# Performance work log

Measured on AMD Instinct MI355X. Metric: run time of the kernel, lower is better.

## Reference

```python
import jax, jax.numpy as jnp
from jax import lax
import numpy as np

H = 128          # hidden_dim
VOCAB = 200000   # word_dim
L = 32           # words per node
NUM_LEAVES = 2048
NUM_PARENTS = 2047
MAXC = 4         # max child slots in a tree row
NCLASS = 4


def setup_inputs() -> dict:
    key = jax.random.key(0)
    ks = jax.random.split(key, 16)
    N = NUM_LEAVES + NUM_PARENTS
    x_word = jax.random.uniform(ks[0], (N, L), dtype=jnp.float32)
    x_index = jax.random.randint(ks[1], (N, L), 0, VOCAB)
    # caterpillar tree: parent idx has one leaf child and the previous parent
    idx = np.arange(NUM_PARENTS)
    tree = np.full((NUM_PARENTS, MAXC), -1, dtype=np.int32)
    tree[:, 0] = idx
    tree[:, 1] = np.where(idx > 0, NUM_LEAVES + idx - 1, NUM_LEAVES - 1)
    tree = jnp.asarray(tree)
    y = jax.random.uniform(ks[2], (NCLASS,), dtype=jnp.float32)
    def init(k, shp):
        return 0.1 * jax.random.normal(k, shp, dtype=jnp.float32)
    return dict(
        x_word=x_word, x_index=x_index, tree=tree, y=y,
        E_bu=init(ks[3], (H, VOCAB)),
        WQ=init(ks[4], (H, H)), WK=init(ks[5], (H, H)), WV=init(ks[6], (H, H)),
        W_z=init(ks[7], (H, H)), U_z=init(ks[8], (H, H)), b_z=jnp.zeros((H,), jnp.float32),
        W_r=init(ks[9], (H, H)), U_r=init(ks[10], (H, H)), b_r=jnp.zeros((H,), jnp.float32),
        W_h=init(ks[11], (H, H)), U_h=init(ks[12], (H, H)), b_h=jnp.zeros((H,), jnp.float32),
        W_out=init(ks[13], (NCLASS, H)), b_out=jnp.zeros((NCLASS,), jnp.float32),
    )


def _forward(x_word, y, E_bu, WQ, WK, WV, W_z, U_z, b_z, W_r, U_r, b_r,
             W_h, U_h, b_h, W_out, b_out, x_index, tree):
    Hd = E_bu.shape[0]
    # parent_xe for every node: weighted sum of embedding columns  [N, H]
    emb = E_bu.T[x_index]                        # [N, L, H] gather
    xe = jnp.einsum('nlh,nl->nh', emb, x_word)
    n_parents = tree.shape[0]
    n_leaves = x_word.shape[0] - n_parents

    def cell(xe_i, h_tilde):
        # W.mul(v).sum(dim=1) == W @ v in the torch code
        z = jax.nn.sigmoid(W_z @ xe_i + U_z @ h_tilde + b_z)
        r = jax.nn.sigmoid(W_r @ xe_i + U_r @ h_tilde + b_r)
        c = jnp.tanh(W_h @ xe_i + U_h @ (h_tilde * r) + b_h)
        return z * h_tilde + (1.0 - z) * c

    # leaves: child_h == 0  =>  h_tilde == 0 (vectorized over all leaves)
    xe_leaf = xe[:n_leaves]
    z_l = jax.nn.sigmoid(xe_leaf @ W_z.T + b_z)
    c_l = jnp.tanh(xe_leaf @ W_h.T + b_h)
    leaf_h = (1.0 - z_l) * c_l

    node_h0 = jnp.zeros((x_word.shape[0], Hd), xe.dtype).at[:n_leaves].set(leaf_h)
    scale = 1.0 / jnp.sqrt(jnp.asarray(Hd, xe.dtype))

    def step(node_h, inp):
        xe_p, row, i = inp
        mask = row >= 0
        child_h = node_h[jnp.clip(row, 0)]                  # [MAXC, H]
        query = jax.nn.sigmoid(xe_p @ WQ)                   # sigmoid(xe @ WQ)
        keyv = child_h @ WK
        val = child_h @ WV
        scores = jnp.where(mask, (query * scale * keyv).sum(-1), -1e9)
        attn = jax.nn.softmax(scores)                       # over children
        h_tilde = attn @ val
        h = cell(xe_p, h_tilde)
        return node_h.at[i].set(h), h

    idxs = jnp.arange(n_parents) + n_leaves
    _, parent_hs = lax.scan(step, node_h0, (xe[n_leaves:], tree, idxs))
    root = parent_hs[-1]
    pred = jax.nn.softmax(W_out @ root + b_out)
    loss = jnp.sum((y - pred) ** 2)
    return pred, loss


def reference(x_word, x_index, tree, y, E_bu, WQ, WK, WV, W_z, U_z, b_z,
              W_r, U_r, b_r, W_h, U_h, b_h, W_out, b_out):
    return _forward(x_word, y, E_bu, WQ, WK, WV, W_z, U_z, b_z, W_r, U_r, b_r,
                    W_h, U_h, b_h, W_out, b_out, x_index, tree)
```

## Files before the change

kernel.cpp:

```cpp
#include <hip/hip_runtime.h>
#include <math.h>

#define HD 128
#define LW 32
#define VOCABN 200000
#define NLEAF 2048
#define NPAR 2047
#define NNODE 4095
#define MAXC 4
#define NCLASS 4
#define SCALE 0.08838834764831845f

#define OFF_XE   0
#define OFF_NODE 524160
#define OFF_W3   786304
#define OFF_WQ   851840
#define OFF_AZ   1113856
#define OFF_AR   1375872
#define OFF_AH   1637888
#define OFF_PREV 1899904
#define OFF_ES   2685952
#define OFF_HG   2688000
#define OFF_HTR  2688128
#define OFF_ET   2688256
#define WS_END   (OFF_ET + (size_t)VOCABN * HD)

#define BARL() asm volatile("s_waitcnt lgkmcnt(0)\n\ts_barrier" ::: "memory")
#define PIN4(v) asm volatile("" : "+v"((v).x), "+v"((v).y), "+v"((v).z), "+v"((v).w))
#define LD4(p, k) (*(const float4*)((p) + 4 * (k)))

typedef __attribute__((ext_vector_type(16))) float fx16;

#define CH(W, X, n4) { a0 += (W).x * (X)[4*(n4)+0] + (W).y * (X)[4*(n4)+1]; \
                       a1 += (W).z * (X)[4*(n4)+2] + (W).w * (X)[4*(n4)+3]; }

#define PIN_ALL() do { PIN4(A0); PIN4(A1); PIN4(A2); PIN4(A3); \
    PIN4(A4); PIN4(A5); PIN4(A6); PIN4(A7); PIN4(A8); PIN4(A9); \
    PIN4(A10); PIN4(A11); PIN4(A12); PIN4(A13); PIN4(A14); PIN4(A15); } while (0)

__global__ void k_xe(const float* __restrict__ xw, const int* __restrict__ xi,
                     const float* __restrict__ E, float* __restrict__ xe) {
    int n = blockIdx.x;
    int h = threadIdx.x;
    __shared__ int   sidx[LW];
    __shared__ float sw[LW];
    if (h < LW) { sidx[h] = xi[n * LW + h]; sw[h] = xw[n * LW + h]; }
    __syncthreads();
    float acc = 0.f;
#pragma unroll
    for (int l = 0; l < LW; ++l)
        acc += E[(size_t)h * VOCABN + sidx[l]] * sw[l];
    xe[(size_t)n * HD + h] = acc;
}

__global__ void k_transpose(const float* __restrict__ E, float* __restrict__ ET) {
    __shared__ float tile[32][33];
    int vb = blockIdx.x * 32, hb = blockIdx.y * 32;
    int tx = threadIdx.x, ty = threadIdx.y;
#pragma unroll
    for (int r = 0; r < 32; r += 8)
        tile[ty + r][tx] = E[(size_t)(hb + ty + r) * VOCABN + vb + tx];
    __syncthreads();
#pragma unroll
    for (int r = 0; r < 32; r += 8)
        ET[(size_t)(vb + ty + r) * HD + hb + tx] = tile[tx][ty + r];
}

__global__ void k_xe_t(const float* __restrict__ xw, const int* __restrict__ xi,
                       const float* __restrict__ ET, float* __restrict__ xe) {
    int n = blockIdx.x;
    int h = threadIdx.x;
    __shared__ int   sidx[LW];
    __shared__ float sw[LW];
    if (h < LW) { sidx[h] = xi[n * LW + h]; sw[h] = xw[n * LW + h]; }
    __syncthreads();
    float acc = 0.f;
#pragma unroll
    for (int l = 0; l < LW; ++l)
        acc += ET[(size_t)sidx[l] * HD + h] * sw[l];
    xe[(size_t)n * HD + h] = acc;
}

__global__ void k_leaf(const float* __restrict__ xe, const float* __restrict__ Wz,
                       const float* __restrict__ bz, const float* __restrict__ Wh,
                       const float* __restrict__ bh, float* __restrict__ node_h) {
    int n = blockIdx.x;
    int j = threadIdx.x;
    __shared__ float xl[HD];
    xl[j] = xe[(size_t)n * HD + j];
    __syncthreads();
    float az = bz[j], ah = bh[j];
    const float* wzr = Wz + (size_t)j * HD;
    const float* whr = Wh + (size_t)j * HD;
#pragma unroll 4
    for (int k = 0; k < HD; ++k) { az += wzr[k] * xl[k]; ah += whr[k] * xl[k]; }
    float z = 1.f / (1.f + expf(-az));
    float c = tanhf(ah);
    node_h[(size_t)n * HD + j] = (1.f - z) * c;
}

__global__ void k_fuse(const float* __restrict__ WV, const float* __restrict__ Uz,
                       const float* __restrict__ Ur, const float* __restrict__ Uh,
                       float* __restrict__ w3) {
    int r = blockIdx.x;
    int b = threadIdx.x;
    float v;
    if (r < 128) {
        v = WV[(size_t)b * HD + r];
    } else if (r < 384) {
        const float* u  = (r < 256 ? Uz + (size_t)(r - 128) * HD : Ur + (size_t)(r - 256) * HD);
        const float* wv = WV + (size_t)b * HD;
        float a = 0.f;
#pragma unroll 4
        for (int j = 0; j < HD; ++j) a += u[j] * wv[j];
        v = a;
    } else {
        v = Uh[(size_t)(r - 384) * HD + b];
    }
    w3[(size_t)r * HD + b] = v;
}

__global__ void k_ppre(const float* __restrict__ xe, const float* __restrict__ WQ,
                       const float* __restrict__ WK, const float* __restrict__ Wz,
                       const float* __restrict__ bz, const float* __restrict__ Wr,
                       const float* __restrict__ br, const float* __restrict__ Wh,
                       const float* __restrict__ bh, float* __restrict__ wq,
                       float* __restrict__ az, float* __restrict__ ar,
                       float* __restrict__ ah) {
    int i = blockIdx.x;
    int j = threadIdx.x;
    __shared__ float xl[HD], ql[HD];
    xl[j] = xe[(size_t)(NLEAF + i) * HD + j];
    __syncthreads();
    float q = 0.f;
#pragma unroll 4
    for (int h = 0; h < HD; ++h) q += xl[h] * WQ[(size_t)h * HD + j];
    ql[j] = 1.f / (1.f + expf(-q));
    __syncthreads();
    float w = 0.f;
#pragma unroll 4
    for (int k = 0; k < HD; ++k) w += WK[(size_t)j * HD + k] * ql[k];
    wq[(size_t)i * HD + j] = w;
    float vz = bz[j], vr = br[j], vh = bh[j];
#pragma unroll 4
    for (int k = 0; k < HD; ++k) {
        float xv = xl[k];
        vz += Wz[(size_t)j * HD + k] * xv;
        vr += Wr[(size_t)j * HD + k] * xv;
        vh += Wh[(size_t)j * HD + k] * xv;
    }
    az[(size_t)i * HD + j] = vz;
    ar[(size_t)i * HD + j] = vr;
    ah[(size_t)i * HD + j] = vh;
}

__global__ void k_chpre(const int* __restrict__ tree, const float* __restrict__ node_h,
                        const float* __restrict__ w3, const float* __restrict__ wq_all,
                        float* __restrict__ preVexp, float* __restrict__ expsum) {
    int i = blockIdx.x;
    int j = threadIdx.x;
    __shared__ float hl[HD];
    __shared__ float red[HD];
    float wqj = wq_all[(size_t)i * HD + j];
    float acc0 = 0.f, acc1 = 0.f, acc2 = 0.f, esum = 0.f;
    for (int c = 0; c < MAXC; ++c) {
        int child = tree[i * MAXC + c];
        if (child < 0 || child >= NLEAF) continue;
        __syncthreads();
        hl[j] = node_h[(size_t)child * HD + j];
        __syncthreads();
        red[j] = hl[j] * wqj;
        __syncthreads();
        for (int s = 64; s > 0; s >>= 1) {
            if (j < s) red[j] += red[j + s];
            __syncthreads();
        }
        float e = expf(red[0] * SCALE);
        float d0 = 0.f, d1 = 0.f, d2 = 0.f;
#pragma unroll 4
        for (int k = 0; k < HD; ++k) {
            float x = hl[k];
            d0 += w3[(size_t)j * HD + k] * x;
            d1 += w3[(size_t)(128 + j) * HD + k] * x;
            d2 += w3[(size_t)(256 + j) * HD + k] * x;
        }
        acc0 += e * d0; acc1 += e * d1; acc2 += e * d2; esum += e;
    }
    preVexp[(size_t)i * 384 + j]       = acc0;
    preVexp[(size_t)i * 384 + 128 + j] = acc1;
    preVexp[(size_t)i * 384 + 256 + j] = acc2;
    if (j == 0) expsum[i] = esum;
}

__global__ __launch_bounds__(1024)
__attribute__((amdgpu_waves_per_eu(4, 4)))
void k_seq(float* __restrict__ ws, const float* __restrict__ Wout,
           const float* __restrict__ bout, const float* __restrict__ y,
           float* __restrict__ out) {
    const int t  = threadIdx.x;
    const int l  = t & 63;
    const int w  = t >> 6;
    const bool isP1 = (w < 12);
    const int q1   = w & 1;
    const int row1 = 64 * (w >> 1) + l;
    const int w12  = w - 12;
    const int q3   = w12 & 1;
    const int row3 = 64 * (w12 >> 1) + l;

    __shared__ float part1[768];
    __shared__ float part3[256];
    __shared__ float sPart[2];
    __shared__ float h_lds[HD];
    __shared__ float outv[NCLASS];

    const int woff = isP1 ? (row1 * HD + 64 * q1)
                          : ((384 + row3) * HD + 64 * q3);
    const float* wp = ws + OFF_W3 + woff;
    float4 A0 = LD4(wp, 0),  A1 = LD4(wp, 1),  A2 = LD4(wp, 2),  A3 = LD4(wp, 3),
           A4 = LD4(wp, 4),  A5 = LD4(wp, 5),  A6 = LD4(wp, 6),  A7 = LD4(wp, 7),
           A8 = LD4(wp, 8),  A9 = LD4(wp, 9),  A10 = LD4(wp, 10), A11 = LD4(wp, 11),
           A12 = LD4(wp, 12), A13 = LD4(wp, 13), A14 = LD4(wp, 14), A15 = LD4(wp, 15);
    PIN_ALL();

    const int xoff = isP1 ? (OFF_HG + 64 * q1) : (OFF_HTR + 64 * q3);
    const float* xp = ws + __builtin_amdgcn_readfirstlane(xoff);

    float pv0 = 0.f, pv1 = 0.f, pv2 = 0.f, paz = 0.f, par = 0.f, pah = 0.f,
          pwq = 0.f, pes = 0.f;
    if (t < HD) {
        pv0 = ws[OFF_PREV + t];       pv1 = ws[OFF_PREV + 128 + t];
        pv2 = ws[OFF_PREV + 256 + t];
        paz = ws[OFF_AZ + t];         par = ws[OFF_AR + t];
        pah = ws[OFF_AH + t];
        pwq = ws[OFF_WQ + HD + t];
        pes = ws[OFF_ES];
        ws[OFF_HG + t] = 0.f;
    }
    if (t < 2) sPart[t] = (t == 0) ? -1e30f : 0.f;
    asm volatile("s_waitcnt vmcnt(0)" ::: "memory");
    __syncthreads();

    float zreg = 0.f, htreg = 0.f, hfin = 0.f, cur_pah = 0.f, cur_pwq = 0.f;

    for (int i = 0; i < NPAR; ++i) {
        const int inext = (i + 1 < NPAR) ? i + 1 : NPAR - 1;
        const int in2   = (i + 2 < NPAR) ? i + 2 : NPAR - 1;

        PIN_ALL();

        if (isP1) {
            fx16 x0, x1, x2, x3;
            asm volatile(
                "s_dcache_inv\n\t"
                "s_load_dwordx16 %0, %4, 0x0\n\t"
                "s_load_dwordx16 %1, %4, 0x40\n\t"
                "s_load_dwordx16 %2, %4, 0x80\n\t"
                "s_load_dwordx16 %3, %4, 0xC0\n\t"
                "s_waitcnt lgkmcnt(0)"
                : "=s"(x0), "=s"(x1), "=s"(x2), "=s"(x3)
                : "s"(xp));
            float a0 = 0.f, a1 = 0.f;
            CH(A0, x0, 0)  CH(A1, x0, 1)  CH(A2, x0, 2)  CH(A3, x0, 3)
            CH(A4, x1, 0)  CH(A5, x1, 1)  CH(A6, x1, 2)  CH(A7, x1, 3)
            CH(A8, x2, 0)  CH(A9, x2, 1)  CH(A10, x2, 2) CH(A11, x2, 3)
            CH(A12, x3, 0) CH(A13, x3, 1) CH(A14, x3, 2) CH(A15, x3, 3)
            part1[q1 * 384 + row1] = a0 + a1;
        }
        BARL();

        if (t < HD) {
            float vdot = part1[t]       + part1[384 + t];
            float zdot = part1[128 + t] + part1[512 + t];
            float rdot = part1[256 + t] + part1[640 + t];
            float sc   = sPart[0] + sPart[1];
            float e    = expf(sc);
            float inv  = 1.f / (pes + e);
            float htv  = (pv0 + e * vdot) * inv;
            float z    = 1.f / (1.f + expf(-(paz + (pv1 + e * zdot) * inv)));
            float rr   = 1.f / (1.f + expf(-(par + (pv2 + e * rdot) * inv)));
            ws[OFF_HTR + t] = htv * rr;
            zreg = z; htreg = htv;
            asm volatile("s_waitcnt vmcnt(0)" ::: "memory");
            cur_pah = pah; cur_pwq = pwq;
            pv0 = ws[OFF_PREV + inext * 384 + t];
            pv1 = ws[OFF_PREV + inext * 384 + 128 + t];
            pv2 = ws[OFF_PREV + inext * 384 + 256 + t];
            paz = ws[OFF_AZ + inext * HD + t];
            par = ws[OFF_AR + inext * HD + t];
            pah = ws[OFF_AH + inext * HD + t];
            pes = ws[OFF_ES + inext];
            pwq = ws[OFF_WQ + in2 * HD + t];
        }
        BARL();

        if (!isP1) {
            fx16 x0, x1, x2, x3;
            asm volatile(
                "s_dcache_inv\n\t"
                "s_load_dwordx16 %0, %4, 0x0\n\t"
                "s_load_dwordx16 %1, %4, 0x40\n\t"
                "s_load_dwordx16 %2, %4, 0x80\n\t"
                "s_load_dwordx16 %3, %4, 0xC0\n\t"
                "s_waitcnt lgkmcnt(0)"
                : "=s"(x0), "=s"(x1), "=s"(x2), "=s"(x3)
                : "s"(xp));
            float a0 = 0.f, a1 = 0.f;
            CH(A0, x0, 0)  CH(A1, x0, 1)  CH(A2, x0, 2)  CH(A3, x0, 3)
            CH(A4, x1, 0)  CH(A5, x1, 1)  CH(A6, x1, 2)  CH(A7, x1, 3)
            CH(A8, x2, 0)  CH(A9, x2, 1)  CH(A10, x2, 2) CH(A11, x2, 3)
            CH(A12, x3, 0) CH(A13, x3, 1) CH(A14, x3, 2) CH(A15, x3, 3)
            part3[q3 * 128 + row3] = a0 + a1;
        }
        BARL();

        if (t < HD) {
            float u  = part3[t] + part3[128 + t];
            float c  = tanhf(cur_pah + u);
            float hv = zreg * htreg + (1.f - zreg) * c;
            hfin = hv;
            ws[OFF_HG + t] = hv;
            float prod = hv * cur_pwq;
#pragma unroll
            for (int o = 32; o > 0; o >>= 1) prod += __shfl_down(prod, o, 64);
            if (l == 0) sPart[w] = prod * SCALE;
            asm volatile("s_waitcnt vmcnt(0)" ::: "memory");
        }
        BARL();
    }

    if (t < HD) h_lds[t] = hfin;
    __syncthreads();
    if (t < NCLASS) {
        float acc = bout[t];
#pragma unroll 4
        for (int k = 0; k < HD; ++k) acc += Wout[(size_t)t * HD + k] * h_lds[k];
        outv[t] = acc;
    }
    __syncthreads();
    if (t == 0) {
        float m  = fmaxf(fmaxf(outv[0], outv[1]), fmaxf(outv[2], outv[3]));
        float e0 = expf(outv[0] - m), e1 = expf(outv[1] - m);
        float e2 = expf(outv[2] - m), e3 = expf(outv[3] - m);
        float inv = 1.f / (e0 + e1 + e2 + e3);
        float p0 = e0 * inv, p1 = e1 * inv, p2 = e2 * inv, p3 = e3 * inv;
        out[0] = p0; out[1] = p1; out[2] = p2; out[3] = p3;
        float d0 = y[0] - p0, d1 = y[1] - p1, d2 = y[2] - p2, d3 = y[3] - p3;
        out[4] = d0 * d0 + d1 * d1 + d2 * d2 + d3 * d3;
    }
}

extern "C" void kernel_launch(void* const* d_in, const int* in_sizes, int n_in,
                              void* d_out, int out_size, void* d_ws, size_t ws_size,
                              hipStream_t stream) {
    const float* x_word  = (const float*)d_in[0];
    const int*   x_index = (const int*)d_in[1];
    const int*   tree    = (const int*)d_in[2];
    const float* y       = (const float*)d_in[3];
    const float* E_bu    = (const float*)d_in[4];
    const float* WQ      = (const float*)d_in[5];
    const float* WK      = (const float*)d_in[6];
    const float* WV      = (const float*)d_in[7];
    const float* W_z     = (const float*)d_in[8];
    const float* U_z     = (const float*)d_in[9];
    const float* b_z     = (const float*)d_in[10];
    const float* W_r     = (const float*)d_in[11];
    const float* U_r     = (const float*)d_in[12];
    const float* b_r     = (const float*)d_in[13];
    const float* W_h     = (const float*)d_in[14];
    const float* U_h     = (const float*)d_in[15];
    const float* b_h     = (const float*)d_in[16];
    const float* W_out   = (const float*)d_in[17];
    const float* b_out   = (const float*)d_in[18];

    float* ws      = (float*)d_ws;
    float* xe      = ws + OFF_XE;
    float* node_h  = ws + OFF_NODE;
    float* w3      = ws + OFF_W3;
    float* wq      = ws + OFF_WQ;
    float* az      = ws + OFF_AZ;
    float* ar      = ws + OFF_AR;
    float* ah      = ws + OFF_AH;
    float* preVexp = ws + OFF_PREV;
    float* expsum  = ws + OFF_ES;
    float* ET      = ws + OFF_ET;

    bool use_transpose = ws_size >= WS_END * sizeof(float);

    if (use_transpose) {
        dim3 tg(VOCABN / 32, HD / 32), tb(32, 8);
        k_transpose<<<tg, tb, 0, stream>>>(E_bu, ET);
        k_xe_t<<<NNODE, HD, 0, stream>>>(x_word, x_index, ET, xe);
    } else {
        k_xe<<<NNODE, HD, 0, stream>>>(x_word, x_index, E_bu, xe);
    }
    k_leaf<<<NLEAF, HD, 0, stream>>>(xe, W_z, b_z, W_h, b_h, node_h);
    k_fuse<<<512, HD, 0, stream>>>(WV, U_z, U_r, U_h, w3);
    k_ppre<<<NPAR, HD, 0, stream>>>(xe, WQ, WK, W_z, b_z, W_r, b_r, W_h, b_h,
                                    wq, az, ar, ah);
    k_chpre<<<NPAR, HD, 0, stream>>>(tree, node_h, w3, wq, preVexp, expsum);
    k_seq<<<1, 1024, 0, stream>>>(ws, W_out, b_out, y, (float*)d_out);
}
```

Before: 4.234 ms.

## Exchange recurrent state through LDS instead of global memory and scalar loads

The per-step vectors h and h_tilde*r now live in shared memory and are read with vector LDS loads. Previously they were written to global workspace and read back with s_dcache_inv plus scalar loads, which needed vmcnt waits. The score reduction is also split: the final phase now only writes the elementwise products to LDS. A spare wave (w==12), idle during phase 1, does the cross-wave reduction in parallel with the P1 matvec. This targets the global-memory round-trip latency on the serial critical path of every step, at the cost of LDS bandwidth and broadcast reads across all lanes.

```diff
diff --git a/kernel.cpp b/kernel.cpp
--- a/kernel.cpp
+++ b/kernel.cpp
@@ -29,10 +29,8 @@
 #define PIN4(v) asm volatile("" : "+v"((v).x), "+v"((v).y), "+v"((v).z), "+v"((v).w))
 #define LD4(p, k) (*(const float4*)((p) + 4 * (k)))
 
-typedef __attribute__((ext_vector_type(16))) float fx16;
-
-#define CH(W, X, n4) { a0 += (W).x * (X)[4*(n4)+0] + (W).y * (X)[4*(n4)+1]; \
-                       a1 += (W).z * (X)[4*(n4)+2] + (W).w * (X)[4*(n4)+3]; }
+#define CHV(W, X) { a0 += (W).x * (X).x + (W).y * (X).y; \
+                    a1 += (W).z * (X).z + (W).w * (X).w; }
 
 #define PIN_ALL() do { PIN4(A0); PIN4(A1); PIN4(A2); PIN4(A3); \
     PIN4(A4); PIN4(A5); PIN4(A6); PIN4(A7); PIN4(A8); PIN4(A9); \
@@ -209,8 +207,10 @@
 
     __shared__ float part1[768];
     __shared__ float part3[256];
-    __shared__ float sPart[2];
-    __shared__ float h_lds[HD];
+    __shared__ float red[HD];
+    __shared__ float sScore;
+    __shared__ __attribute__((aligned(16))) float h_lds[HD];
+    __shared__ __attribute__((aligned(16))) float htr_lds[HD];
     __shared__ float outv[NCLASS];
 
     const int woff = isP1 ? (row1 * HD + 64 * q1)
@@ -222,8 +222,8 @@
            A12 = LD4(wp, 12), A13 = LD4(wp, 13), A14 = LD4(wp, 14), A15 = LD4(wp, 15);
     PIN_ALL();
 
-    const int xoff = isP1 ? (OFF_HG + 64 * q1) : (OFF_HTR + 64 * q3);
-    const float* xp = ws + __builtin_amdgcn_readfirstlane(xoff);
+    const float4* xb1 = (const float4*)(h_lds   + 64 * q1);
+    const float4* xb3 = (const float4*)(htr_lds + 64 * q3);
 
     float pv0 = 0.f, pv1 = 0.f, pv2 = 0.f, paz = 0.f, par = 0.f, pah = 0.f,
           pwq = 0.f, pes = 0.f;
@@ -234,10 +234,9 @@
         pah = ws[OFF_AH + t];
         pwq = ws[OFF_WQ + HD + t];
         pes = ws[OFF_ES];
-        ws[OFF_HG + t] = 0.f;
-    }
-    if (t < 2) sPart[t] = (t == 0) ? -1e30f : 0.f;
-    asm volatile("s_waitcnt vmcnt(0)" ::: "memory");
+        h_lds[t] = 0.f;
+        red[t]   = -1e30f;
+    }
     __syncthreads();
 
     float zreg = 0.f, htreg = 0.f, hfin = 0.f, cur_pah = 0.f, cur_pwq = 0.f;
@@ -249,22 +248,21 @@
         PIN_ALL();
 
         if (isP1) {
-            fx16 x0, x1, x2, x3;
-            asm volatile(
-                "s_dcache_inv\n\t"
-                "s_load_dwordx16 %0, %4, 0x0\n\t"
-                "s_load_dwordx16 %1, %4, 0x40\n\t"
-                "s_load_dwordx16 %2, %4, 0x80\n\t"
-                "s_load_dwordx16 %3, %4, 0xC0\n\t"
-                "s_waitcnt lgkmcnt(0)"
-                : "=s"(x0), "=s"(x1), "=s"(x2), "=s"(x3)
-                : "s"(xp));
+            float4 X0 = xb1[0], X1 = xb1[1], X2 = xb1[2], X3 = xb1[3];
+            float4 X4 = xb1[4], X5 = xb1[5], X6 = xb1[6], X7 = xb1[7];
             float a0 = 0.f, a1 = 0.f;
-            CH(A0, x0, 0)  CH(A1, x0, 1)  CH(A2, x0, 2)  CH(A3, x0, 3)
-            CH(A4, x1, 0)  CH(A5, x1, 1)  CH(A6, x1, 2)  CH(A7, x1, 3)
-            CH(A8, x2, 0)  CH(A9, x2, 1)  CH(A10, x2, 2) CH(A11, x2, 3)
-            CH(A12, x3, 0) CH(A13, x3, 1) CH(A14, x3, 2) CH(A15, x3, 3)
+            CHV(A0, X0) CHV(A1, X1) CHV(A2, X2) CHV(A3, X3)
+            X0 = xb1[8]; X1 = xb1[9]; X2 = xb1[10]; X3 = xb1[11];
+            CHV(A4, X4) CHV(A5, X5) CHV(A6, X6) CHV(A7, X7)
+            X4 = xb1[12]; X5 = xb1[13]; X6 = xb1[14]; X7 = xb1[15];
+            CHV(A8, X0) CHV(A9, X1) CHV(A10, X2) CHV(A11, X3)
+            CHV(A12, X4) CHV(A13, X5) CHV(A14, X6) CHV(A15, X7)
             part1[q1 * 384 + row1] = a0 + a1;
+        } else if (w == 12) {
+            float s = red[l] + red[l + 64];
+#pragma unroll
+            for (int o = 32; o > 0; o >>= 1) s += __shfl_down(s, o, 64);
+            if (l == 0) sScore = s * SCALE;
         }
         BARL();
 
@@ -272,15 +270,13 @@
             float vdot = part1[t]       + part1[384 + t];
             float zdot = part1[128 + t] + part1[512 + t];
             float rdot = part1[256 + t] + part1[640 + t];
-            float sc   = sPart[0] + sPart[1];
-            float e    = expf(sc);
+            float e    = expf(sScore);
             float inv  = 1.f / (pes + e);
             float htv  = (pv0 + e * vdot) * inv;
             float z    = 1.f / (1.f + expf(-(paz + (pv1 + e * zdot) * inv)));
             float rr   = 1.f / (1.f + expf(-(par + (pv2 + e * rdot) * inv)));
-            ws[OFF_HTR + t] = htv * rr;
+            htr_lds[t] = htv * rr;
             zreg = z; htreg = htv;
-            asm volatile("s_waitcnt vmcnt(0)" ::: "memory");
             cur_pah = pah; cur_pwq = pwq;
             pv0 = ws[OFF_PREV + inext * 384 + t];
             pv1 = ws[OFF_PREV + inext * 384 + 128 + t];
@@ -294,21 +290,15 @@
         BARL();
 
         if (!isP1) {
-            fx16 x0, x1, x2, x3;
-            asm volatile(
-                "s_dcache_inv\n\t"
-                "s_load_dwordx16 %0, %4, 0x0\n\t"
-                "s_load_dwordx16 %1, %4, 0x40\n\t"
-                "s_load_dwordx16 %2, %4, 0x80\n\t"
-                "s_load_dwordx16 %3, %4, 0xC0\n\t"
-                "s_waitcnt lgkmcnt(0)"
-                : "=s"(x0), "=s"(x1), "=s"(x2), "=s"(x3)
-                : "s"(xp));
+            float4 X0 = xb3[0], X1 = xb3[1], X2 = xb3[2], X3 = xb3[3];
+            float4 X4 = xb3[4], X5 = xb3[5], X6 = xb3[6], X7 = xb3[7];
             float a0 = 0.f, a1 = 0.f;
-            CH(A0, x0, 0)  CH(A1, x0, 1)  CH(A2, x0, 2)  CH(A3, x0, 3)
-            CH(A4, x1, 0)  CH(A5, x1, 1)  CH(A6, x1, 2)  CH(A7, x1, 3)
-            CH(A8, x2, 0)  CH(A9, x2, 1)  CH(A10, x2, 2) CH(A11, x2, 3)
-            CH(A12, x3, 0) CH(A13, x3, 1) CH(A14, x3, 2) CH(A15, x3, 3)
+            CHV(A0, X0) CHV(A1, X1) CHV(A2, X2) CHV(A3, X3)
+            X0 = xb3[8]; X1 = xb3[9]; X2 = xb3[10]; X3 = xb3[11];
+            CHV(A4, X4) CHV(A5, X5) CHV(A6, X6) CHV(A7, X7)
+            X4 = xb3[12]; X5 = xb3[13]; X6 = xb3[14]; X7 = xb3[15];
+            CHV(A8, X0) CHV(A9, X1) CHV(A10, X2) CHV(A11, X3)
+            CHV(A12, X4) CHV(A13, X5) CHV(A14, X6) CHV(A15, X7)
             part3[q3 * 128 + row3] = a0 + a1;
         }
         BARL();
@@ -318,18 +308,12 @@
             float c  = tanhf(cur_pah + u);
             float hv = zreg * htreg + (1.f - zreg) * c;
             hfin = hv;
-            ws[OFF_HG + t] = hv;
-            float prod = hv * cur_pwq;
-#pragma unroll
-            for (int o = 32; o > 0; o >>= 1) prod += __shfl_down(prod, o, 64);
-            if (l == 0) sPart[w] = prod * SCALE;
-            asm volatile("s_waitcnt vmcnt(0)" ::: "memory");
+            h_lds[t] = hv;
+            red[t]   = hv * cur_pwq;
         }
         BARL();
     }
 
-    if (t < HD) h_lds[t] = hfin;
-    __syncthreads();
     if (t < NCLASS) {
         float acc = bout[t];
 #pragma unroll 4
```

Result: slower. 4.854 ms (+14.6%).
